# Kernel tuning notes

Measured on AMD Instinct MI355X. Metric: run time of the kernel, lower is better.

## Reference

```python
import jax, jax.numpy as jnp
import numpy as np

H = 64  # hidden_size


def _lstm_layer(x_tbi, W_ih, W_hh, b_ih, b_hh):
    """x_tbi: [T, B, I] time-major. Returns [T, B, H]. PyTorch gate order i,f,g,o."""
    T, B, _ = x_tbi.shape
    # Precompute input contribution for all timesteps in one big GEMM.
    gx = jnp.einsum('tbi,gi->tbg', x_tbi, W_ih) + b_ih + b_hh  # [T, B, 4H]

    def step(carry, gx_t):
        h, c = carry
        g = gx_t + h @ W_hh.T  # [B, 4H]
        i, f, gg, o = jnp.split(g, 4, axis=-1)
        i = jax.nn.sigmoid(i)
        f = jax.nn.sigmoid(f)
        gg = jnp.tanh(gg)
        o = jax.nn.sigmoid(o)
        c = f * c + i * gg
        h = o * jnp.tanh(c)
        return (h, c), h

    h0 = jnp.zeros((B, H), dtype=x_tbi.dtype)
    c0 = jnp.zeros((B, H), dtype=x_tbi.dtype)
    _, hs = jax.lax.scan(step, (h0, c0), gx)
    return hs  # [T, B, H]


def setup_inputs() -> dict:
    key = jax.random.key(0)
    ks = jax.random.split(key, 20)
    B, T, I = 4096, 256, 32
    s_in = 1.0 / np.sqrt(H)  # PyTorch LSTM init scale
    d = {
        'x': jax.random.normal(ks[0], (B, T, I), jnp.float32),
        'W_ih0': jax.random.uniform(ks[1], (4 * H, I), jnp.float32, -s_in, s_in),
        'W_hh0': jax.random.uniform(ks[2], (4 * H, H), jnp.float32, -s_in, s_in),
        'b_ih0': jax.random.uniform(ks[3], (4 * H,), jnp.float32, -s_in, s_in),
        'b_hh0': jax.random.uniform(ks[4], (4 * H,), jnp.float32, -s_in, s_in),
        'W_ih1': jax.random.uniform(ks[5], (4 * H, H), jnp.float32, -s_in, s_in),
        'W_hh1': jax.random.uniform(ks[6], (4 * H, H), jnp.float32, -s_in, s_in),
        'b_ih1': jax.random.uniform(ks[7], (4 * H,), jnp.float32, -s_in, s_in),
        'b_hh1': jax.random.uniform(ks[8], (4 * H,), jnp.float32, -s_in, s_in),
        'W_ih2': jax.random.uniform(ks[9], (4 * H, H), jnp.float32, -s_in, s_in),
        'W_hh2': jax.random.uniform(ks[10], (4 * H, H), jnp.float32, -s_in, s_in),
        'b_ih2': jax.random.uniform(ks[11], (4 * H,), jnp.float32, -s_in, s_in),
        'b_hh2': jax.random.uniform(ks[12], (4 * H,), jnp.float32, -s_in, s_in),
        'fc1_w': jax.random.uniform(ks[13], (32, H), jnp.float32, -s_in, s_in),
        'fc1_b': jax.random.uniform(ks[14], (32,), jnp.float32, -s_in, s_in),
        'fc2_w': jax.random.uniform(ks[15], (1, 32), jnp.float32, -1.0 / np.sqrt(32), 1.0 / np.sqrt(32)),
        'fc2_b': jax.random.uniform(ks[16], (1,), jnp.float32, -1.0 / np.sqrt(32), 1.0 / np.sqrt(32)),
    }
    return d


def reference(x, W_ih0, W_hh0, b_ih0, b_hh0, W_ih1, W_hh1, b_ih1, b_hh1,
              W_ih2, W_hh2, b_ih2, b_hh2, fc1_w, fc1_b, fc2_w, fc2_b):
    # Eval-mode forward (dropout between LSTM layers and before fc1 is identity).
    h = jnp.transpose(x, (1, 0, 2))  # [T, B, I] time-major
    h = _lstm_layer(h, W_ih0, W_hh0, b_ih0, b_hh0)
    h = _lstm_layer(h, W_ih1, W_hh1, b_ih1, b_hh1)
    h = _lstm_layer(h, W_ih2, W_hh2, b_ih2, b_hh2)
    last = h[-1]  # [B, H] == out[:, -1, :]
    z = jax.nn.relu(last @ fc1_w.T + fc1_b)
    return z @ fc2_w.T + fc2_b  # [B, 1]
```

## Files before the change

kernel.cpp:

```cpp
#include <hip/hip_runtime.h>

typedef __attribute__((ext_vector_type(8))) short bf16x8;
typedef __attribute__((ext_vector_type(4))) float f32x4;

#define HID 64
#define TSTEPS 256
#define BATCH 4096
#define BT 16
#define RST 1024
#define XOFF  0
#define H0OFF 256
#define H1OFF 512
#define H2OFF 768

__device__ __forceinline__ float frcp(float x){ return __builtin_amdgcn_rcpf(x); }
__device__ __forceinline__ float fexp2(float x){ return __builtin_amdgcn_exp2f(x); }

__device__ __forceinline__ void lds_barrier(){
  asm volatile("s_waitcnt lgkmcnt(0)\n\ts_barrier" ::: "memory");
}

__device__ __forceinline__ ushort f2bf(float f){
  unsigned u = __float_as_uint(f);
  u += 0x7fff + ((u>>16)&1);
  return (ushort)(u>>16);
}
__device__ __forceinline__ float bf2f(ushort u){ return __uint_as_float(((unsigned)u)<<16); }
__device__ __forceinline__ unsigned cvtpk(float lo, float hi){
  unsigned r;
  asm("v_cvt_pk_bf16_f32 %0, %1, %2" : "=v"(r) : "v"(lo), "v"(hi));
  return r;
}

__device__ __forceinline__ void load_wb_rt(const float* __restrict__ Wih,
    const float* __restrict__ Whh, const float* __restrict__ bih,
    const float* __restrict__ bhh, int IN, bf16x8 (&wf)[4][4], f32x4 (&bvv)[4],
    int s, int l15, int lhi){
  const float L2E = 1.4426950408889634f;
  const int nk = (IN + 64) >> 5;
  #pragma unroll
  for (int g = 0; g < 4; ++g){
    const float sc = (g == 2) ? 2.f*L2E : L2E;
    int n = g*64 + s*16 + l15;
    #pragma unroll
    for (int r = 0; r < 4; ++r){
      int nr = g*64 + s*16 + lhi*4 + r;
      bvv[g][r] = (bih[nr] + bhh[nr]) * sc;
    }
    #pragma unroll
    for (int kt = 0; kt < 4; ++kt){
      if (kt < nk){
        int kb = kt*32 + lhi*8;
        const float* src = (kb < IN) ? (Wih + (size_t)n*IN + kb)
                                     : (Whh + (size_t)n*64 + (kb - IN));
        bf16x8 v;
        #pragma unroll
        for (int j = 0; j < 8; ++j) v[j] = (short)f2bf(src[j] * sc);
        wf[kt][g] = v;
      }
    }
  }
}

__device__ __forceinline__ void ew4(const f32x4 (&A)[4], float (&cst)[4],
                                    unsigned &p01, unsigned &p23){
  float h[4];
  #pragma unroll
  for (int r = 0; r < 4; ++r){
    float Ai = fexp2(-A[0][r]);
    float Bf = fexp2(-A[1][r]);
    float G  = fexp2( A[2][r]);
    float O  = fexp2(-A[3][r]);
    float a1 = 1.f + Ai, b1 = 1.f + Bf, gp = G + 1.f, gm = G - 1.f;
    float cp = (cst[r]*a1*gp + b1*gm) * frcp(a1*b1*gp);
    cst[r] = cp;
    float C2 = fexp2(cp * 2.8853900817779268f);
    h[r] = (C2 - 1.f) * frcp((1.f + O)*(C2 + 1.f));
  }
  p01 = cvtpk(h[0], h[1]);
  p23 = cvtpk(h[2], h[3]);
}

template<int SL, bool L0, bool L1, bool L2>
__device__ __forceinline__ void diag_step(char* lds, int d, int lw,
    const bf16x8 (&wf)[4][4], const f32x4 (&bvv)[4], float (&cst)[4],
    float2 &xr, const float* __restrict__ xbase,
    int aIn, int aRec, int wH, int xwAddr){
  const int RSo = (SL^1)*128;
  const int SLo = SL*128;
  const bool act = (lw == 0) ? L0 : ((lw == 1) ? L1 : L2);

  if (act){
    if (lw == 0){
      unsigned pk = cvtpk(xr.x, xr.y);
      *reinterpret_cast<unsigned*>(lds + xwAddr + RSo) = pk;
      int tn = d + 2; if (tn > TSTEPS-1) tn = TSTEPS-1;
      xr = *reinterpret_cast<const float2*>(xbase + (size_t)tn*32);
    }

    bf16x8 t0, t1, t2, t3;
    if (lw == 0){
      t0 = *reinterpret_cast<const bf16x8*>(lds + aIn + SLo);
      t1 = *reinterpret_cast<const bf16x8*>(lds + aRec + RSo);
      t2 = *reinterpret_cast<const bf16x8*>(lds + (aRec^64) + RSo);
    } else {
      t0 = *reinterpret_cast<const bf16x8*>(lds + aIn + RSo);
      t1 = *reinterpret_cast<const bf16x8*>(lds + (aIn^64) + RSo);
      t2 = *reinterpret_cast<const bf16x8*>(lds + aRec + RSo);
      t3 = *reinterpret_cast<const bf16x8*>(lds + (aRec^64) + RSo);
    }
    f32x4 A[4];
    __builtin_amdgcn_s_setprio(1);
    #pragma unroll
    for (int g = 0; g < 4; ++g){
      f32x4 c = bvv[g];
      c = __builtin_amdgcn_mfma_f32_16x16x32_bf16(wf[0][g], t0, c, 0, 0, 0);
      c = __builtin_amdgcn_mfma_f32_16x16x32_bf16(wf[1][g], t1, c, 0, 0, 0);
      A[g] = __builtin_amdgcn_mfma_f32_16x16x32_bf16(wf[2][g], t2, c, 0, 0, 0);
    }
    if (lw != 0){
      #pragma unroll
      for (int g = 0; g < 4; ++g)
        A[g] = __builtin_amdgcn_mfma_f32_16x16x32_bf16(wf[3][g], t3, A[g], 0, 0, 0);
    }
    __builtin_amdgcn_s_setprio(0);

    unsigned p01, p23;
    ew4(A, cst, p01, p23);
    *reinterpret_cast<uint2*>(lds + wH + SLo) = make_uint2(p01, p23);
  }
  lds_barrier();
}

__global__ __launch_bounds__(768, 1) void lstm3_wave_kernel(
    const float* __restrict__ x,
    const float* Wih0, const float* Whh0, const float* bih0, const float* bhh0,
    const float* Wih1, const float* Whh1, const float* bih1, const float* bhh1,
    const float* Wih2, const float* Whh2, const float* bih2, const float* bhh2,
    const float* __restrict__ fc1w, const float* __restrict__ fc1b,
    const float* __restrict__ fc2w, const float* __restrict__ fc2b,
    float* __restrict__ out){
  __shared__ char lds[BT*RST];
  __shared__ float fcbuf[BT*16];

  const int tid  = threadIdx.x;
  const int lane = tid & 63;
  const int wid  = tid >> 6;
  const int s    = wid & 3;
  const int lw   = wid >> 2;
  const int l15  = lane & 15;
  const int lhi  = lane >> 4;
  const int row0 = blockIdx.x * BT;

  const float* Wih = (lw == 0) ? Wih0 : ((lw == 1) ? Wih1 : Wih2);
  const float* Whh = (lw == 0) ? Whh0 : ((lw == 1) ? Whh1 : Whh2);
  const float* bih = (lw == 0) ? bih0 : ((lw == 1) ? bih1 : bih2);
  const float* bhh = (lw == 0) ? bhh0 : ((lw == 1) ? bhh1 : bhh2);
  const int IN = (lw == 0) ? 32 : 64;

  bf16x8 wf[4][4];
  f32x4 bvv[4];
  load_wb_rt(Wih, Whh, bih, bhh, IN, wf, bvv, s, l15, lhi);

  const int rdA  = l15*RST + ((lhi*16) ^ ((l15 & 7) << 4));
  const int aIn  = rdA + ((lw == 0) ? XOFF : ((lw == 1) ? H0OFF : H1OFF));
  const int aRec = rdA + (H0OFF + lw*256);
  const int wH = l15*RST + (H0OFF + lw*256) + ((s*32 + lhi*8) ^ ((l15 & 7) << 4));
  const int xrow = (tid & 255) >> 4;
  const int xwAddr = xrow*RST + XOFF + (((tid & 15)*4) ^ ((xrow & 7) << 4));
  const float* xbase = x + ((size_t)(row0 + xrow)*TSTEPS)*32 + (tid & 15)*2;

  *reinterpret_cast<int4*>(lds + tid*16) = make_int4(0, 0, 0, 0);
  if (tid < 256)
    *reinterpret_cast<int4*>(lds + 12288 + tid*16) = make_int4(0, 0, 0, 0);
  __syncthreads();
  float2 xr = make_float2(0.f, 0.f);
  if (tid < 256){
    float2 v0 = *reinterpret_cast<const float2*>(xbase);
    *reinterpret_cast<unsigned*>(lds + xwAddr) = cvtpk(v0.x, v0.y);
    xr = *reinterpret_cast<const float2*>(xbase + 32);
  }
  __syncthreads();

  float cst[4] = {0.f, 0.f, 0.f, 0.f};

  #define ARGS lds, d, lw, wf, bvv, cst, xr, xbase, aIn, aRec, wH, xwAddr
  { int d = 0; diag_step<0, true, false, false>(ARGS); }
  { int d = 1; diag_step<1, true, true,  false>(ARGS); }
  for (int d = 2; d < 256; d += 2){
    diag_step<0, true, true, true>(ARGS);
    ++d;
    diag_step<1, true, true, true>(ARGS);
    --d;
  }
  { int d = 256; diag_step<0, false, true,  true>(ARGS); }
  { int d = 257; diag_step<1, false, false, true>(ARGS); }
  #undef ARGS

  __syncthreads();

  if (tid < 256){
    const int row  = tid & 15;
    const int slot = tid >> 4;
    const int rx   = (row & 7) << 4;
    float hv[HID];
    #pragma unroll
    for (int i = 0; i < HID; ++i)
      hv[i] = bf2f(*reinterpret_cast<const ushort*>(
                   lds + row*RST + (H2OFF + 128) + ((i*2) ^ rx)));
    float p = 0.f;
    #pragma unroll
    for (int jj = 0; jj < 2; ++jj){
      int j = slot*2 + jj;
      float z = fc1b[j];
      #pragma unroll
      for (int i = 0; i < HID; ++i) z += hv[i]*fc1w[j*HID + i];
      z = fmaxf(z, 0.f);
      p += z * fc2w[j];
    }
    fcbuf[row*16 + slot] = p;
  }
  __syncthreads();
  if (tid < BT){
    float s2 = fc2b[0];
    #pragma unroll
    for (int k = 0; k < 16; ++k) s2 += fcbuf[tid*16 + k];
    out[row0 + tid] = s2;
  }
}

extern "C" void kernel_launch(void* const* d_in, const int* in_sizes, int n_in,
                              void* d_out, int out_size, void* d_ws, size_t ws_size,
                              hipStream_t stream){
  const float* x    = (const float*)d_in[0];
  const float* Wih0 = (const float*)d_in[1];
  const float* Whh0 = (const float*)d_in[2];
  const float* bih0 = (const float*)d_in[3];
  const float* bhh0 = (const float*)d_in[4];
  const float* Wih1 = (const float*)d_in[5];
  const float* Whh1 = (const float*)d_in[6];
  const float* bih1 = (const float*)d_in[7];
  const float* bhh1 = (const float*)d_in[8];
  const float* Wih2 = (const float*)d_in[9];
  const float* Whh2 = (const float*)d_in[10];
  const float* bih2 = (const float*)d_in[11];
  const float* bhh2 = (const float*)d_in[12];
  const float* fc1w = (const float*)d_in[13];
  const float* fc1b = (const float*)d_in[14];
  const float* fc2w = (const float*)d_in[15];
  const float* fc2b = (const float*)d_in[16];

  lstm3_wave_kernel<<<BATCH/BT, 768, 0, stream>>>(x,
      Wih0, Whh0, bih0, bhh0,
      Wih1, Whh1, bih1, bhh1,
      Wih2, Whh2, bih2, bhh2,
      fc1w, fc1b, fc2w, fc2b, (float*)d_out);
}
```

Before: 278.5 us.

## Replace block barriers with per-wave LDS flag polling and triple buffering

Replaces the per-diagonal-step workgroup barrier with point-to-point readiness flags in LDS: each wave polls the write flags of the producer waves before reading and the read flags of the consumer waves before overwriting. The LDS state moves from double to triple buffering (row stride grows) so producers can run one step ahead without clobbering data still being read. The aim is to let the three layer wavefronts drift relative to each other instead of lock-stepping all 12 waves on every step. In exchange it adds spin loops with s_sleep, volatile LDS flag traffic and extra LDS footprint, and its correctness depends on LDS memory ordering between waves.

```diff
diff --git a/kernel.cpp b/kernel.cpp
--- a/kernel.cpp
+++ b/kernel.cpp
@@ -7,18 +7,10 @@
 #define TSTEPS 256
 #define BATCH 4096
 #define BT 16
-#define RST 1024
-#define XOFF  0
-#define H0OFF 256
-#define H1OFF 512
-#define H2OFF 768
+#define RST 1536
 
 __device__ __forceinline__ float frcp(float x){ return __builtin_amdgcn_rcpf(x); }
 __device__ __forceinline__ float fexp2(float x){ return __builtin_amdgcn_exp2f(x); }
-
-__device__ __forceinline__ void lds_barrier(){
-  asm volatile("s_waitcnt lgkmcnt(0)\n\ts_barrier" ::: "memory");
-}
 
 __device__ __forceinline__ ushort f2bf(float f){
   unsigned u = __float_as_uint(f);
@@ -30,6 +22,23 @@
   unsigned r;
   asm("v_cvt_pk_bf16_f32 %0, %1, %2" : "=v"(r) : "v"(lo), "v"(hi));
   return r;
+}
+
+__device__ __forceinline__ void poll4(volatile int* p, int tgt){
+  for(;;){
+    int m0 = p[0], m1 = p[1], m2 = p[2], m3 = p[3];
+    if (min(min(m0,m1),min(m2,m3)) >= tgt) break;
+    __builtin_amdgcn_s_sleep(1);
+  }
+}
+__device__ __forceinline__ void poll8(volatile int* p, int tgt){
+  for(;;){
+    int m0 = p[0], m1 = p[1], m2 = p[2], m3 = p[3];
+    int m4 = p[4], m5 = p[5], m6 = p[6], m7 = p[7];
+    int m = min(min(min(m0,m1),min(m2,m3)), min(min(m4,m5),min(m6,m7)));
+    if (m >= tgt) break;
+    __builtin_amdgcn_s_sleep(1);
+  }
 }
 
 __device__ __forceinline__ void load_wb_rt(const float* __restrict__ Wih,
@@ -81,33 +90,42 @@
   p23 = cvtpk(h[2], h[3]);
 }
 
-template<int SL, bool L0, bool L1, bool L2>
-__device__ __forceinline__ void diag_step(char* lds, int d, int lw,
+template<int S>
+__device__ __forceinline__ void diag_iter(char* lds, volatile int* wfl, volatile int* rfl,
+    int d, int lw, int s, int lane,
     const bf16x8 (&wf)[4][4], const f32x4 (&bvv)[4], float (&cst)[4],
     float2 &xr, const float* __restrict__ xbase,
-    int aIn, int aRec, int wH, int xwAddr){
-  const int RSo = (SL^1)*128;
-  const int SLo = SL*128;
-  const bool act = (lw == 0) ? L0 : ((lw == 1) ? L1 : L2);
-
-  if (act){
+    int rdA, int wHbase, int xwAddr, int aInBase, int aRecBase){
+  constexpr int RS = (S+2)%3;
+  constexpr int XS = (S+1)%3;
+  const bool active = (unsigned)(d - lw) <= 255u;
+
+  if (lw > 0) poll8(wfl + (lw-1)*4, d-1);
+  else        poll4(wfl, d-1);
+  asm volatile("" ::: "memory");
+
+  bf16x8 t0, t1, t2, t3;
+  if (active){
     if (lw == 0){
-      unsigned pk = cvtpk(xr.x, xr.y);
-      *reinterpret_cast<unsigned*>(lds + xwAddr + RSo) = pk;
-      int tn = d + 2; if (tn > TSTEPS-1) tn = TSTEPS-1;
+      t0 = *reinterpret_cast<const bf16x8*>(lds + S*128 + rdA);
+      t1 = *reinterpret_cast<const bf16x8*>(lds + aRecBase + RS*128 + rdA);
+      t2 = *reinterpret_cast<const bf16x8*>(lds + aRecBase + RS*128 + (rdA^64));
+    } else {
+      t0 = *reinterpret_cast<const bf16x8*>(lds + aInBase  + RS*128 + rdA);
+      t1 = *reinterpret_cast<const bf16x8*>(lds + aInBase  + RS*128 + (rdA^64));
+      t2 = *reinterpret_cast<const bf16x8*>(lds + aRecBase + RS*128 + rdA);
+      t3 = *reinterpret_cast<const bf16x8*>(lds + aRecBase + RS*128 + (rdA^64));
+    }
+  }
+  asm volatile("s_waitcnt lgkmcnt(0)" ::: "memory");
+  if (lane == 0) rfl[lw*4 + s] = d;
+
+  unsigned xpk = 0, p01 = 0, p23 = 0;
+  if (active){
+    if (lw == 0){
+      xpk = cvtpk(xr.x, xr.y);
+      int tn = d + 2; if (tn > 255) tn = 255;
       xr = *reinterpret_cast<const float2*>(xbase + (size_t)tn*32);
-    }
-
-    bf16x8 t0, t1, t2, t3;
-    if (lw == 0){
-      t0 = *reinterpret_cast<const bf16x8*>(lds + aIn + SLo);
-      t1 = *reinterpret_cast<const bf16x8*>(lds + aRec + RSo);
-      t2 = *reinterpret_cast<const bf16x8*>(lds + (aRec^64) + RSo);
-    } else {
-      t0 = *reinterpret_cast<const bf16x8*>(lds + aIn + RSo);
-      t1 = *reinterpret_cast<const bf16x8*>(lds + (aIn^64) + RSo);
-      t2 = *reinterpret_cast<const bf16x8*>(lds + aRec + RSo);
-      t3 = *reinterpret_cast<const bf16x8*>(lds + (aRec^64) + RSo);
     }
     f32x4 A[4];
     __builtin_amdgcn_s_setprio(1);
@@ -124,12 +142,20 @@
         A[g] = __builtin_amdgcn_mfma_f32_16x16x32_bf16(wf[3][g], t3, A[g], 0, 0, 0);
     }
     __builtin_amdgcn_s_setprio(0);
-
-    unsigned p01, p23;
     ew4(A, cst, p01, p23);
-    *reinterpret_cast<uint2*>(lds + wH + SLo) = make_uint2(p01, p23);
-  }
-  lds_barrier();
+  }
+
+  if (lw < 2) poll8(rfl + lw*4, d-2);
+  else        poll4(rfl + 2*4, d-2);
+  asm volatile("" ::: "memory");
+
+  if (active){
+    if (lw == 0)
+      *reinterpret_cast<unsigned*>(lds + XS*128 + xwAddr) = xpk;
+    *reinterpret_cast<uint2*>(lds + wHbase + S*128) = make_uint2(p01, p23);
+  }
+  asm volatile("s_waitcnt lgkmcnt(0)" ::: "memory");
+  if (lane == 0) wfl[lw*4 + s] = d;
 }
 
 __global__ __launch_bounds__(768, 1) void lstm3_wave_kernel(
@@ -141,6 +167,8 @@
     const float* __restrict__ fc2w, const float* __restrict__ fc2b,
     float* __restrict__ out){
   __shared__ char lds[BT*RST];
+  __shared__ int wfl[12];
+  __shared__ int rfl[12];
   __shared__ float fcbuf[BT*16];
 
   const int tid  = threadIdx.x;
@@ -162,17 +190,18 @@
   f32x4 bvv[4];
   load_wb_rt(Wih, Whh, bih, bhh, IN, wf, bvv, s, l15, lhi);
 
-  const int rdA  = l15*RST + ((lhi*16) ^ ((l15 & 7) << 4));
-  const int aIn  = rdA + ((lw == 0) ? XOFF : ((lw == 1) ? H0OFF : H1OFF));
-  const int aRec = rdA + (H0OFF + lw*256);
-  const int wH = l15*RST + (H0OFF + lw*256) + ((s*32 + lhi*8) ^ ((l15 & 7) << 4));
+  const int rdA = l15*RST + ((lhi*16) ^ ((l15 & 7) << 4));
+  const int aInBase  = (lw == 1) ? 384 : 768;
+  const int aRecBase = 384 + lw*384;
+  const int wHbase = l15*RST + (384 + lw*384) +
+                     ((s*32 + lhi*8) ^ ((l15 & 7) << 4));
   const int xrow = (tid & 255) >> 4;
-  const int xwAddr = xrow*RST + XOFF + (((tid & 15)*4) ^ ((xrow & 7) << 4));
+  const int xwAddr = xrow*RST + (((tid & 15)*4) ^ ((xrow & 7) << 4));
   const float* xbase = x + ((size_t)(row0 + xrow)*TSTEPS)*32 + (tid & 15)*2;
 
   *reinterpret_cast<int4*>(lds + tid*16) = make_int4(0, 0, 0, 0);
-  if (tid < 256)
-    *reinterpret_cast<int4*>(lds + 12288 + tid*16) = make_int4(0, 0, 0, 0);
+  *reinterpret_cast<int4*>(lds + 12288 + tid*16) = make_int4(0, 0, 0, 0);
+  if (tid < 12){ wfl[tid] = -1; rfl[tid] = -1; }
   __syncthreads();
   float2 xr = make_float2(0.f, 0.f);
   if (tid < 256){
@@ -184,18 +213,15 @@
 
   float cst[4] = {0.f, 0.f, 0.f, 0.f};
 
-  #define ARGS lds, d, lw, wf, bvv, cst, xr, xbase, aIn, aRec, wH, xwAddr
-  { int d = 0; diag_step<0, true, false, false>(ARGS); }
-  { int d = 1; diag_step<1, true, true,  false>(ARGS); }
-  for (int d = 2; d < 256; d += 2){
-    diag_step<0, true, true, true>(ARGS);
-    ++d;
-    diag_step<1, true, true, true>(ARGS);
-    --d;
-  }
-  { int d = 256; diag_step<0, false, true,  true>(ARGS); }
-  { int d = 257; diag_step<1, false, false, true>(ARGS); }
-  #undef ARGS
+  for (int k = 0; k < 86; ++k){
+    int d = 3*k;
+    diag_iter<0>(lds, wfl, rfl, d,   lw, s, lane, wf, bvv, cst, xr, xbase,
+                 rdA, wHbase, xwAddr, aInBase, aRecBase);
+    diag_iter<1>(lds, wfl, rfl, d+1, lw, s, lane, wf, bvv, cst, xr, xbase,
+                 rdA, wHbase, xwAddr, aInBase, aRecBase);
+    diag_iter<2>(lds, wfl, rfl, d+2, lw, s, lane, wf, bvv, cst, xr, xbase,
+                 rdA, wHbase, xwAddr, aInBase, aRecBase);
+  }
 
   __syncthreads();
 
@@ -207,7 +233,7 @@
     #pragma unroll
     for (int i = 0; i < HID; ++i)
       hv[i] = bf2f(*reinterpret_cast<const ushort*>(
-                   lds + row*RST + (H2OFF + 128) + ((i*2) ^ rx)));
+                   lds + row*RST + 1408 + ((i*2) ^ rx)));
     float p = 0.f;
     #pragma unroll
     for (int jj = 0; jj < 2; ++jj){
```

Result: slower. 457.2 us (+64.2%).
